# Kernel tuning notes

Measured on AMD Instinct MI355X. Metric: run time of the kernel, lower is better.

## Reference

```python
import jax, jax.numpy as jnp
import numpy as np

T, B, N = 512, 256, 128


def setup_inputs() -> dict:
    key = jax.random.key(0)
    k1, k2, k3, k4, k5, k6 = jax.random.split(key, 6)
    emit = jax.random.normal(k1, (T, B, N), dtype=jnp.float32)
    target = jax.random.randint(k2, (T, B), 0, N)
    # prefix-true mask from random lengths in [1, T]
    lengths = jax.random.randint(k3, (B,), 1, T + 1)
    mask = jnp.arange(T)[:, None] < lengths[None, :]
    std = (1.0 / N) ** 0.5
    trans = jax.random.normal(k4, (N, N), dtype=jnp.float32) * std
    strans = jax.random.normal(k5, (N,), dtype=jnp.float32) * std
    etrans = jax.random.normal(k6, (N,), dtype=jnp.float32) * std
    return {"emit": emit, "target": target, "mask": mask,
            "trans": trans, "strans": strans, "etrans": etrans}


def _logZ(emit, mask, trans, strans, etrans):
    alpha0 = strans + emit[0]  # (B, N)

    def step(alpha, xs):
        e_t, m_t = xs  # (B, N), (B,)
        # scores[b, j] = logsumexp_i(alpha[b, i] + trans[i, j] + e_t[b, j])
        scores = jax.scipy.special.logsumexp(
            alpha[:, :, None] + trans[None, :, :] + e_t[:, None, :], axis=1)
        alpha = jnp.where(m_t[:, None], scores, alpha)
        return alpha, None

    alpha, _ = jax.lax.scan(step, alpha0, (emit[1:], mask[1:]))
    return jax.scipy.special.logsumexp(alpha + etrans, axis=1).sum()


def _score(emit, target, mask, trans, strans, etrans):
    Tn, Bn, _ = emit.shape
    # emission scores of gold tags: (T, B)
    sc = jnp.take_along_axis(emit, target[:, :, None], axis=2)[..., 0]
    # transition scores between consecutive gold tags
    sc = sc.at[1:].add(trans[target[:-1], target[1:]])
    score = jnp.sum(jnp.where(mask, sc, jnp.float32(0.0)))
    ends = mask.astype(jnp.int32).sum(axis=0) - 1  # (B,)
    score = score + strans[target[0]].sum()
    score = score + etrans[target[ends, jnp.arange(Bn)]].sum()
    return score


def reference(emit, target, mask, trans, strans, etrans):
    Bn = emit.shape[1]
    logZ = _logZ(emit, mask, trans, strans, etrans)
    score = _score(emit, target, mask, trans, strans, etrans)
    return (logZ - score) / Bn
```

## Files before the change

kernel.cpp:

```cpp
#include <hip/hip_runtime.h>

#define TT 512
#define BB 256
#define NN 128
#define MW 16
#define NWG (BB / MW)
#define STH 144
#define GRID (32 + TT)

#define LENS_OFF 256
#define AF_OFF 2048
#define CF_OFF (AF_OFF + BB * NN * 4)
#define BU_OFF (CF_OFF + 1024)
#define CB_OFF (BU_OFF + BB * NN * 4)
#define WS_NEED ((size_t)CB_OFF + 1024)

typedef __attribute__((ext_vector_type(8))) short short8_t;
typedef __attribute__((ext_vector_type(4))) float f32x4;

__device__ __forceinline__ unsigned short f2bf(float f) {
  unsigned u = __float_as_uint(f);
  return (unsigned short)((u + 0x7FFF + ((u >> 16) & 1)) >> 16);
}
__device__ __forceinline__ float bf2f(unsigned short h) {
  return __uint_as_float(((unsigned)h) << 16);
}
__device__ __forceinline__ int orig_j(int p) {
  return 32 * (p >> 5) + 16 * (p & 1) + ((p >> 1) & 15);
}
__device__ __forceinline__ unsigned pk_bf16(float a, float b) {
  unsigned r;
  asm("v_cvt_pk_bf16_f32 %0, %1, %2" : "=v"(r) : "v"(a), "v"(b));
  return r;
}

#define BARRIER_LGKM() \
  asm volatile("s_waitcnt lgkmcnt(0)\n\ts_barrier" ::: "memory")

template <bool FWD>
__device__ __forceinline__ void step_one(
    int T_, bool NORM, const float* __restrict__ emit,
    unsigned short (&sVg)[2][MW * STH], int (&nrmg)[2][MW], int& nb,
    int (&cloc)[4], const int (&lm1)[4], const int (&off8)[8],
    float (&RL)[8], const float (&RO)[8], const float (&XU)[8],
    float (&XF)[8], const short8_t (&eB)[4][2], float eet0, float eet1,
    int w, int c, int qd, bool nwriter) {
  const int POUT = T_ & 1, PIN = POUT ^ 1;
  {
    int tl = FWD ? (T_ + 2 < TT ? T_ + 2 : TT - 1) : (T_ - 2 > 0 ? T_ - 2 : 0);
    const size_t gb = (size_t)tl * (BB * NN);
#pragma unroll
    for (int i = 0; i < 8; ++i) RL[i] = emit[gb + off8[i]];
  }
  const short8_t A0 = *(const short8_t*)&sVg[PIN][c * STH + 0 + qd * 8];
  const short8_t A1 = *(const short8_t*)&sVg[PIN][c * STH + 32 + qd * 8];
  const short8_t A2 = *(const short8_t*)&sVg[PIN][c * STH + 64 + qd * 8];
  const short8_t A3 = *(const short8_t*)&sVg[PIN][c * STH + 96 + qd * 8];
  f32x4 p0 = {0.f, 0.f, 0.f, 0.f}, q0 = {0.f, 0.f, 0.f, 0.f};
  f32x4 p1 = {0.f, 0.f, 0.f, 0.f}, q1 = {0.f, 0.f, 0.f, 0.f};
  p0 = __builtin_amdgcn_mfma_f32_16x16x32_bf16(A0, eB[0][0], p0, 0, 0, 0);
  p1 = __builtin_amdgcn_mfma_f32_16x16x32_bf16(A0, eB[0][1], p1, 0, 0, 0);
  q0 = __builtin_amdgcn_mfma_f32_16x16x32_bf16(A2, eB[2][0], q0, 0, 0, 0);
  q1 = __builtin_amdgcn_mfma_f32_16x16x32_bf16(A2, eB[2][1], q1, 0, 0, 0);
  p0 = __builtin_amdgcn_mfma_f32_16x16x32_bf16(A1, eB[1][0], p0, 0, 0, 0);
  p1 = __builtin_amdgcn_mfma_f32_16x16x32_bf16(A1, eB[1][1], p1, 0, 0, 0);
  q0 = __builtin_amdgcn_mfma_f32_16x16x32_bf16(A3, eB[3][0], q0, 0, 0, 0);
  q1 = __builtin_amdgcn_mfma_f32_16x16x32_bf16(A3, eB[3][1], q1, 0, 0, 0);
#pragma unroll
  for (int i = 0; i < 8; ++i) XF[i] = __expf(RO[i]);
  const f32x4 ac0 = p0 + q0;
  const f32x4 ac1 = p1 + q1;

  if (NORM) {
    const int4 nr = *(const int4*)&nrmg[nb][4 * qd];
    const int nA[4] = {nr.x, nr.y, nr.z, nr.w};
    int nnw[4];
#pragma unroll
    for (int r_ = 0; r_ < 4; ++r_) {
      float v0, v1;
      if (FWD) {
        v0 = ldexpf(ac0[r_] * XU[2 * r_], -nA[r_]);
        v1 = ldexpf(ac1[r_] * XU[2 * r_ + 1], -nA[r_]);
        if (T_ <= lm1[r_]) {
          *(unsigned*)&sVg[POUT][(4 * qd + r_) * STH + 32 * w + 2 * c] =
              pk_bf16(v0, v1);
          cloc[r_] += nA[r_];
        }
      } else {
        const bool isact = (T_ == lm1[r_]);
        v0 = isact ? XU[2 * r_] * eet0 : ldexpf(ac0[r_] * XU[2 * r_], -nA[r_]);
        v1 = isact ? XU[2 * r_ + 1] * eet1
                   : ldexpf(ac1[r_] * XU[2 * r_ + 1], -nA[r_]);
        if (T_ <= lm1[r_]) {
          *(unsigned*)&sVg[POUT][(4 * qd + r_) * STH + 32 * w + 2 * c] =
              pk_bf16(v0, v1);
          cloc[r_] = isact ? 0 : cloc[r_] + nA[r_];
        }
      }
      nnw[r_] = ((int)((__float_as_uint(v0) >> 23) & 0xFF)) - 120;
    }
    if (nwriter)
      *(int4*)&nrmg[nb ^ 1][4 * qd] = make_int4(nnw[0], nnw[1], nnw[2], nnw[3]);
    nb ^= 1;
  } else {
#pragma unroll
    for (int r_ = 0; r_ < 4; ++r_) {
      float v0, v1;
      if (FWD) {
        v0 = ac0[r_] * XU[2 * r_];
        v1 = ac1[r_] * XU[2 * r_ + 1];
        if (T_ <= lm1[r_]) {
          *(unsigned*)&sVg[POUT][(4 * qd + r_) * STH + 32 * w + 2 * c] =
              pk_bf16(v0, v1);
        }
      } else {
        const bool isact = (T_ == lm1[r_]);
        v0 = isact ? XU[2 * r_] * eet0 : ac0[r_] * XU[2 * r_];
        v1 = isact ? XU[2 * r_ + 1] * eet1 : ac1[r_] * XU[2 * r_ + 1];
        if (T_ <= lm1[r_]) {
          *(unsigned*)&sVg[POUT][(4 * qd + r_) * STH + 32 * w + 2 * c] =
              pk_bf16(v0, v1);
          cloc[r_] = isact ? 0 : cloc[r_];
        }
      }
    }
  }
}

__global__ __launch_bounds__(256, 1) void crf_fb8(
    const float* __restrict__ emit, const int* __restrict__ target,
    const void* __restrict__ maskp, const float* __restrict__ trans,
    const float* __restrict__ strans, const float* __restrict__ etrans,
    float* __restrict__ ws, int* __restrict__ lens, float* __restrict__ AF,
    int* __restrict__ CF, float* __restrict__ BU, int* __restrict__ CB) {
  __shared__ __align__(16) unsigned short sV[2][MW * STH];
  __shared__ __align__(16) int nrm[2][MW];
  __shared__ __align__(16) int sC[MW];
  __shared__ int slen[MW];
  __shared__ int smax_s;
  __shared__ float rf[4];

  const int bid = blockIdx.x;
  const int tid = threadIdx.x;
  const unsigned char* mk8 = (const unsigned char*)maskp;
  const int* mk32 = (const int*)maskp;
  const bool is_u8 = (mk8[1] != 0);

  if (bid >= 32) {
    const int b = tid;
    const int t = bid - 32;
    int m = is_u8 ? (mk8[t * BB + b] != 0) : (mk32[t * BB + b] != 0);
    float v = 0.f;
    if (m) {
      int tg = target[t * BB + b];
      v = emit[((size_t)t * BB + b) * NN + tg];
      v += (t > 0) ? trans[target[(t - 1) * BB + b] * NN + tg] : strans[tg];
      int mn = (t + 1 < TT) ? (is_u8 ? (mk8[(t + 1) * BB + b] != 0)
                                     : (mk32[(t + 1) * BB + b] != 0))
                            : 0;
      if (!mn) {
        v += etrans[tg];
        lens[b] = t + 1;
      }
    }
#pragma unroll
    for (int off = 32; off; off >>= 1) v += __shfl_down(v, off, 64);
    if ((b & 63) == 0) rf[b >> 6] = v;
    __syncthreads();
    if (b == 0) atomicAdd(&ws[1], rf[0] + rf[1] + rf[2] + rf[3]);
    return;
  }

  const bool bwd = (bid >= NWG);
  const int g = bwd ? bid - NWG : bid;
  const int bg = g * MW;
  const int w = tid >> 6, l = tid & 63, c = l & 15, qd = l >> 4;

  if (tid == 0) smax_s = 0;
  __syncthreads();
  if (tid < MW) {
    const int b = bg + tid;
    int len = 1;
#pragma unroll
    for (int st = 256; st; st >>= 1) {
      int t2 = len + st;
      if (t2 <= TT) {
        bool mv = is_u8 ? (mk8[(size_t)(t2 - 1) * BB + b] != 0)
                        : (mk32[(size_t)(t2 - 1) * BB + b] != 0);
        if (mv) len = t2;
      }
    }
    slen[tid] = len;
    atomicMax(&smax_s, len);
  }

  short8_t eB[4][2];
#pragma unroll
  for (int kt = 0; kt < 4; ++kt)
#pragma unroll
    for (int u = 0; u < 2; ++u)
#pragma unroll
      for (int jj = 0; jj < 8; ++jj) {
        int kp = kt * 32 + qd * 8 + jj;
        int a_ = orig_j(kp);
        int b_ = 32 * w + 16 * u + c;
        float tv = bwd ? trans[b_ * NN + a_] : trans[a_ * NN + b_];
        eB[kt][u][jj] = (short)f2bf(__expf(tv));
      }
  const float eet0 = __expf(etrans[32 * w + c]);
  const float eet1 = __expf(etrans[32 * w + 16 + c]);

  {
    const int m = tid & 15;
    const int pbase = (tid >> 4) * 8;
    if (!bwd) {
      const int b = bg + m;
#pragma unroll
      for (int pp = 0; pp < 8; ++pp) {
        int p = pbase + pp;
        int j = orig_j(p);
        float v = __expf(strans[j] + emit[(size_t)b * NN + j]);
        sV[0][m * STH + p] = f2bf(v);
        if (p == 0)
          nrm[0][m] = ((int)((__float_as_uint(v) >> 23) & 0xFF)) - 120;
      }
    } else {
#pragma unroll
      for (int pp = 0; pp < 8; ++pp) {
        int p = pbase + pp;
        sV[0][m * STH + p] = 0x3F80;
        sV[1][m * STH + p] = 0x3F80;
        if (p == 0) { nrm[0][m] = 0; nrm[1][m] = 0; }
      }
    }
  }
  __syncthreads();
  const int smax = smax_s;
  int lm1[4];
#pragma unroll
  for (int r = 0; r < 4; ++r) lm1[r] = slen[4 * qd + r] - 1;

  int cloc[4] = {0, 0, 0, 0};
  int nb = 0;
  const bool nwriter = (w == 0 && c == 0);

  int off8[8];
#pragma unroll
  for (int r = 0; r < 4; ++r)
#pragma unroll
    for (int u = 0; u < 2; ++u)
      off8[r * 2 + u] = (bg + 4 * qd + r) * NN + 32 * w + 16 * u + c;

  int NIT, T0;
  if (!bwd) {
    const int LmaxF = (smax < 258) ? smax : 258;
    NIT = LmaxF - 1;
    T0 = 1;
  } else {
    NIT = (smax >= 259) ? smax - 258 : 0;
    T0 = smax - 1;
  }

  if (NIT > 0) {
    float ra[8], rb[8], x0[8], x1[8];
    {
      const int a1 = bwd ? (T0 - 1 > 0 ? T0 - 1 : 0)
                         : (T0 + 1 < TT ? T0 + 1 : TT - 1);
#pragma unroll
      for (int i = 0; i < 8; ++i) {
        ra[i] = emit[(size_t)T0 * (BB * NN) + off8[i]];
        rb[i] = emit[(size_t)a1 * (BB * NN) + off8[i]];
      }
#pragma unroll
      for (int i = 0; i < 8; ++i) x0[i] = __expf(ra[i]);
    }
    if (!bwd) {
      for (int itb = 0; itb < NIT; itb += 4) {
#pragma unroll
        for (int k = 0; k < 4; ++k) {
          const int it = itb + k;
          if (it >= NIT) break;
          if ((k & 1) == 0)
            step_one<true>(T0 + it, k == 3, emit, sV, nrm, nb, cloc, lm1, off8,
                           ra, rb, x0, x1, eB, eet0, eet1, w, c, qd, nwriter);
          else
            step_one<true>(T0 + it, k == 3, emit, sV, nrm, nb, cloc, lm1, off8,
                           rb, ra, x1, x0, eB, eet0, eet1, w, c, qd, nwriter);
          BARRIER_LGKM();
        }
      }
    } else {
      for (int itb = 0; itb < NIT; itb += 4) {
#pragma unroll
        for (int k = 0; k < 4; ++k) {
          const int it = itb + k;
          if (it >= NIT) break;
          if ((k & 1) == 0)
            step_one<false>(T0 - it, k == 3, emit, sV, nrm, nb, cloc, lm1,
                            off8, ra, rb, x0, x1, eB, eet0, eet1, w, c, qd,
                            nwriter);
          else
            step_one<false>(T0 - it, k == 3, emit, sV, nrm, nb, cloc, lm1,
                            off8, rb, ra, x1, x0, eB, eet0, eet1, w, c, qd,
                            nwriter);
          BARRIER_LGKM();
        }
      }
    }
  }

  if (nwriter)
    *(int4*)&sC[4 * qd] = make_int4(cloc[0], cloc[1], cloc[2], cloc[3]);
  __syncthreads();
  {
    const int m = tid >> 4, i16 = tid & 15;
    if (!bwd) {
      int nf = slen[m] - 1;
      if (nf > 257) nf = 257;
      const int pf = nf & 1;
#pragma unroll
      for (int pp = 0; pp < 8; ++pp) {
        int p = i16 * 8 + pp;
        AF[(size_t)(bg + m) * NN + p] = bf2f(sV[pf][m * STH + p]);
      }
      if (i16 == 0) CF[bg + m] = sC[m];
    } else {
#pragma unroll
      for (int pp = 0; pp < 8; ++pp) {
        int p = i16 * 8 + pp;
        BU[(size_t)(bg + m) * NN + p] = bf2f(sV[0][m * STH + p]);
      }
      if (i16 == 0) CB[bg + m] = sC[m];
    }
  }
}

__global__ __launch_bounds__(256) void crf_comb(
    const float* __restrict__ trans, const float* __restrict__ etrans,
    const int* __restrict__ lens, const float* __restrict__ AF,
    const int* __restrict__ CF, const float* __restrict__ BU,
    const int* __restrict__ CB, float* __restrict__ ws,
    float* __restrict__ out) {
  __shared__ __align__(16) unsigned short sU[MW * STH];
  __shared__ float sRed[4][MW][2];
  __shared__ int slen[MW];
  const int tid = threadIdx.x;
  const int w = tid >> 6, l = tid & 63, c = l & 15, qd = l >> 4;
  const int g = blockIdx.x, bg = g * MW;

  if (tid < MW) slen[tid] = lens[bg + tid];
  {
    const int m = tid & 15, pbase = (tid >> 4) * 8;
#pragma unroll
    for (int pp = 0; pp < 8; ++pp) {
      int p = pbase + pp;
      sU[m * STH + p] = f2bf(BU[(size_t)(bg + m) * NN + p]);
    }
  }
  short8_t eB[4][2];
#pragma unroll
  for (int kt = 0; kt < 4; ++kt)
#pragma unroll
    for (int u = 0; u < 2; ++u)
#pragma unroll
      for (int jj = 0; jj < 8; ++jj) {
        int kp = kt * 32 + qd * 8 + jj;
        int a_ = orig_j(kp);
        int b_ = 32 * w + 16 * u + c;
        eB[kt][u][jj] = (short)f2bf(__expf(trans[b_ * NN + a_]));
      }
  const float eet0 = __expf(etrans[32 * w + c]);
  const float eet1 = __expf(etrans[32 * w + 16 + c]);
  __syncthreads();

  const short8_t A0 = *(const short8_t*)&sU[c * STH + 0 + qd * 8];
  const short8_t A1 = *(const short8_t*)&sU[c * STH + 32 + qd * 8];
  const short8_t A2 = *(const short8_t*)&sU[c * STH + 64 + qd * 8];
  const short8_t A3 = *(const short8_t*)&sU[c * STH + 96 + qd * 8];
  f32x4 ac0 = {0.f, 0.f, 0.f, 0.f}, ac1 = {0.f, 0.f, 0.f, 0.f};
  ac0 = __builtin_amdgcn_mfma_f32_16x16x32_bf16(A0, eB[0][0], ac0, 0, 0, 0);
  ac1 = __builtin_amdgcn_mfma_f32_16x16x32_bf16(A0, eB[0][1], ac1, 0, 0, 0);
  ac0 = __builtin_amdgcn_mfma_f32_16x16x32_bf16(A1, eB[1][0], ac0, 0, 0, 0);
  ac1 = __builtin_amdgcn_mfma_f32_16x16x32_bf16(A1, eB[1][1], ac1, 0, 0, 0);
  ac0 = __builtin_amdgcn_mfma_f32_16x16x32_bf16(A2, eB[2][0], ac0, 0, 0, 0);
  ac1 = __builtin_amdgcn_mfma_f32_16x16x32_bf16(A2, eB[2][1], ac1, 0, 0, 0);
  ac0 = __builtin_amdgcn_mfma_f32_16x16x32_bf16(A3, eB[3][0], ac0, 0, 0, 0);
  ac1 = __builtin_amdgcn_mfma_f32_16x16x32_bf16(A3, eB[3][1], ac1, 0, 0, 0);

#pragma unroll
  for (int r_ = 0; r_ < 4; ++r_) {
    float a0 = AF[(size_t)(bg + 4 * qd + r_) * NN + 32 * w + 2 * c];
    float a1 = AF[(size_t)(bg + 4 * qd + r_) * NN + 32 * w + 2 * c + 1];
    float dB = a0 * ac0[r_] + a1 * ac1[r_];
    float dA = a0 * eet0 + a1 * eet1;
#pragma unroll
    for (int mk = 1; mk < 16; mk <<= 1) {
      dB += __shfl_xor(dB, mk, 64);
      dA += __shfl_xor(dA, mk, 64);
    }
    if (c == 0) {
      sRed[w][4 * qd + r_][0] = dB;
      sRed[w][4 * qd + r_][1] = dA;
    }
  }
  __syncthreads();
  if (tid < MW) {
    float DB = sRed[0][tid][0] + sRed[1][tid][0] + sRed[2][tid][0] + sRed[3][tid][0];
    float DA = sRed[0][tid][1] + sRed[1][tid][1] + sRed[2][tid][1] + sRed[3][tid][1];
    const int len = slen[tid];
    const float LN2 = 0.6931471805599453f;
    float logZ;
    if (len >= 259)
      logZ = LN2 * (float)(CF[bg + tid] + CB[bg + tid]) + __logf(DB);
    else
      logZ = LN2 * (float)CF[bg + tid] + __logf(DA);
    atomicAdd(&ws[0], logZ);
  }
  __syncthreads();
  if (tid == 0) {
    __threadfence();
    unsigned old = atomicAdd((unsigned*)ws + 3, 1u);
    if (old == NWG - 1) {
      float zz = atomicAdd(&ws[0], 0.f);
      float ss = atomicAdd(&ws[1], 0.f);
      out[0] = (zz - ss) * (1.0f / (float)BB);
    }
  }
}

__global__ __launch_bounds__(256, 1) void crf_fused_fb(
    const float* __restrict__ emit, const int* __restrict__ target,
    const void* __restrict__ maskp, const float* __restrict__ trans,
    const float* __restrict__ strans, const float* __restrict__ etrans,
    float* __restrict__ ws, float* __restrict__ out) {
  __shared__ __align__(16) unsigned short sV[2][MW * STH];
  __shared__ __align__(16) int nrm[2][MW];
  __shared__ __align__(16) int sC[MW];
  __shared__ int slen[MW];
  __shared__ float sscore;
  __shared__ int smax;

  const int tid = threadIdx.x;
  const int w = tid >> 6;
  const int l = tid & 63;
  const int c = l & 15;
  const int qd = l >> 4;
  const int bg = blockIdx.x * MW;

  if (tid < MW) slen[tid] = 0;
  if (tid == 0) { sscore = 0.f; smax = 0; }
  __syncthreads();

  const unsigned char* mk8 = (const unsigned char*)maskp;
  const int* mk32 = (const int*)maskp;
  const bool is_u8 = (mk8[1] != 0);
  {
    const int mi = tid & 15;
    const int b = bg + mi;
    const int t0 = (tid >> 4) * 32;
    int cnt = 0;
    float sc = 0.f;
    for (int s = 0; s < 32; ++s) {
      int t = t0 + s;
      int m = is_u8 ? (mk8[t * BB + b] != 0) : (mk32[t * BB + b] != 0);
      if (m) {
        cnt++;
        int tg = target[t * BB + b];
        float v = emit[((size_t)t * BB + b) * NN + tg];
        v += (t > 0) ? trans[target[(t - 1) * BB + b] * NN + tg] : strans[tg];
        int mn = (t + 1 < TT) ? (is_u8 ? (mk8[(t + 1) * BB + b] != 0)
                                       : (mk32[(t + 1) * BB + b] != 0))
                              : 0;
        if (!mn) v += etrans[tg];
        sc += v;
      }
    }
    atomicAdd(&slen[mi], cnt);
    atomicAdd(&sscore, sc);
  }

  short8_t eB[4][2];
#pragma unroll
  for (int kt = 0; kt < 4; ++kt)
#pragma unroll
    for (int u = 0; u < 2; ++u)
#pragma unroll
      for (int jj = 0; jj < 8; ++jj) {
        int kp = kt * 32 + qd * 8 + jj;
        int i = orig_j(kp);
        int j = 32 * w + 16 * u + c;
        eB[kt][u][jj] = (short)f2bf(__expf(trans[i * NN + j]));
      }

  {
    const int m = tid & 15;
    const int b = bg + m;
    const int pbase = (tid >> 4) * 8;
#pragma unroll
    for (int pp = 0; pp < 8; ++pp) {
      int p = pbase + pp;
      int j = orig_j(p);
      float v = __expf(strans[j] + emit[(size_t)b * NN + j]);
      sV[0][m * STH + p] = f2bf(v);
      if (p == 0)
        nrm[0][m] = ((int)((__float_as_uint(v) >> 23) & 0xFF)) - 120;
    }
  }
  __syncthreads();

  if (tid < MW) atomicMax(&smax, slen[tid]);
  if (tid == 0) atomicAdd(&ws[1], sscore);
  __syncthreads();
  const int Lmax = smax;
  int lenr[4];
#pragma unroll
  for (int r = 0; r < 4; ++r) lenr[r] = slen[4 * qd + r];

  int off8[8];
#pragma unroll
  for (int r = 0; r < 4; ++r)
#pragma unroll
    for (int u = 0; u < 2; ++u)
      off8[r * 2 + u] = (bg + 4 * qd + r) * NN + 32 * w + 16 * u + c;

  float ra[8], rb[8], xv[8];
  {
#pragma unroll
    for (int i = 0; i < 8; ++i) ra[i] = emit[(size_t)1 * BB * NN + off8[i]];
#pragma unroll
    for (int i = 0; i < 8; ++i) rb[i] = emit[(size_t)2 * BB * NN + off8[i]];
#pragma unroll
    for (int i = 0; i < 8; ++i) xv[i] = __expf(ra[i]);
  }
  int cloc[4] = {0, 0, 0, 0};
  const bool nwriter = (w == 0 && c == 0);

#define CRF_STEP(T_, PIN, POUT, RL, RO)                                       \
  do {                                                                        \
    int tl = ((T_) + 2 < TT) ? (T_) + 2 : TT - 1;                             \
    const size_t gbase = (size_t)tl * (BB * NN);                              \
    _Pragma("unroll") for (int i_ = 0; i_ < 8; ++i_)                          \
        RL[i_] = emit[gbase + off8[i_]];                                      \
    const short8_t A0 = *(const short8_t*)&sV[PIN][c * STH + 0 + qd * 8];     \
    const short8_t A1 = *(const short8_t*)&sV[PIN][c * STH + 32 + qd * 8];    \
    const short8_t A2 = *(const short8_t*)&sV[PIN][c * STH + 64 + qd * 8];    \
    const short8_t A3 = *(const short8_t*)&sV[PIN][c * STH + 96 + qd * 8];    \
    const int4 nr = *(const int4*)&nrm[PIN][4 * qd];                          \
    f32x4 ac0 = {0.f, 0.f, 0.f, 0.f}, ac1 = {0.f, 0.f, 0.f, 0.f};             \
    ac0 = __builtin_amdgcn_mfma_f32_16x16x32_bf16(A0, eB[0][0], ac0, 0, 0, 0);\
    ac1 = __builtin_amdgcn_mfma_f32_16x16x32_bf16(A0, eB[0][1], ac1, 0, 0, 0);\
    ac0 = __builtin_amdgcn_mfma_f32_16x16x32_bf16(A1, eB[1][0], ac0, 0, 0, 0);\
    ac1 = __builtin_amdgcn_mfma_f32_16x16x32_bf16(A1, eB[1][1], ac1, 0, 0, 0);\
    ac0 = __builtin_amdgcn_mfma_f32_16x16x32_bf16(A2, eB[2][0], ac0, 0, 0, 0);\
    ac1 = __builtin_amdgcn_mfma_f32_16x16x32_bf16(A2, eB[2][1], ac1, 0, 0, 0);\
    ac0 = __builtin_amdgcn_mfma_f32_16x16x32_bf16(A3, eB[3][0], ac0, 0, 0, 0);\
    ac1 = __builtin_amdgcn_mfma_f32_16x16x32_bf16(A3, eB[3][1], ac1, 0, 0, 0);\
    const int nA[4] = {nr.x, nr.y, nr.z, nr.w};                               \
    int nnw[4];                                                               \
    _Pragma("unroll") for (int r_ = 0; r_ < 4; ++r_) {                        \
      float y0 = ac0[r_] * xv[2 * r_];                                        \
      float y1 = ac1[r_] * xv[2 * r_ + 1];                                    \
      float v0 = ldexpf(y0, -nA[r_]);                                         \
      float v1 = ldexpf(y1, -nA[r_]);                                         \
      if ((T_) < lenr[r_]) {                                                  \
        unsigned pk = (unsigned)f2bf(v0) | ((unsigned)f2bf(v1) << 16);        \
        *(unsigned*)&sV[POUT][(4 * qd + r_) * STH + 32 * w + 2 * c] = pk;     \
        cloc[r_] += nA[r_];                                                   \
      }                                                                       \
      nnw[r_] = ((int)((__float_as_uint(v0) >> 23) & 0xFF)) - 120;            \
    }                                                                         \
    if (nwriter)                                                              \
      *(int4*)&nrm[POUT][4 * qd] = make_int4(nnw[0], nnw[1], nnw[2], nnw[3]); \
    _Pragma("unroll") for (int i_ = 0; i_ < 8; ++i_)                          \
        xv[i_] = __expf(RO[i_]);                                              \
    __syncthreads();                                                          \
  } while (0)

  for (int t = 1; t < Lmax; t += 2) {
    CRF_STEP(t, 0, 1, ra, rb);
    if (t + 1 < Lmax) {
      CRF_STEP(t + 1, 1, 0, rb, ra);
    }
  }
#undef CRF_STEP

  if (nwriter) *(int4*)&sC[4 * qd] = make_int4(cloc[0], cloc[1], cloc[2], cloc[3]);
  __syncthreads();
  {
    const int m = tid >> 4, i16 = tid & 15;
    const int pb = (slen[m] - 1) & 1;
    float s = 0.f;
#pragma unroll
    for (int pp = 0; pp < 8; ++pp) {
      int p = i16 * 8 + pp;
      int j = orig_j(p);
      s += bf2f(sV[pb][m * STH + p]) * __expf(etrans[j]);
    }
    s += __shfl_xor(s, 1, 64);
    s += __shfl_xor(s, 2, 64);
    s += __shfl_xor(s, 4, 64);
    s += __shfl_xor(s, 8, 64);
    if (i16 == 0)
      atomicAdd(&ws[0], (float)sC[m] * 0.69314718f + __logf(s));
  }
  __syncthreads();
  if (tid == 0) {
    __threadfence();
    unsigned old = atomicAdd((unsigned*)ws + 3, 1u);
    if (old == NWG - 1) {
      float zz = atomicAdd(&ws[0], 0.f);
      float ss = atomicAdd(&ws[1], 0.f);
      out[0] = (zz - ss) * (1.0f / (float)BB);
    }
  }
}

extern "C" void kernel_launch(void* const* d_in, const int* in_sizes, int n_in,
                              void* d_out, int out_size, void* d_ws, size_t ws_size,
                              hipStream_t stream) {
  const float* emit = (const float*)d_in[0];
  const int* target = (const int*)d_in[1];
  const void* mask = (const void*)d_in[2];
  const float* trans = (const float*)d_in[3];
  const float* strans = (const float*)d_in[4];
  const float* etrans = (const float*)d_in[5];
  float* ws = (float*)d_ws;
  float* out = (float*)d_out;

  hipMemsetAsync(d_ws, 0, 16, stream);
  if (ws_size >= WS_NEED) {
    int* lens = (int*)((char*)d_ws + LENS_OFF);
    float* AF = (float*)((char*)d_ws + AF_OFF);
    int* CF = (int*)((char*)d_ws + CF_OFF);
    float* BU = (float*)((char*)d_ws + BU_OFF);
    int* CB = (int*)((char*)d_ws + CB_OFF);
    crf_fb8<<<GRID, 256, 0, stream>>>(emit, target, mask, trans, strans,
                                      etrans, ws, lens, AF, CF, BU, CB);
    crf_comb<<<NWG, 256, 0, stream>>>(trans, etrans, lens, AF, CF, BU, CB, ws,
                                      out);
  } else {
    crf_fused_fb<<<NWG, 256, 0, stream>>>(emit, target, mask, trans, strans,
                                          etrans, ws, out);
  }
}
```

Measured before the change: 231.2 us.

## Deepen emission prefetch to four steps and remove tail branches in recurrence loop

The forward/backward recurrence loop now rotates four emission register buffers, so global loads are issued four timesteps ahead instead of two. The iteration count is rounded up to a multiple of four, which removes the per-step break checks. Extra padded steps are made harmless by clamping the write predicate with lm1 and tmin. The normalization-exponent LDS read is hoisted out of the step function and done before the normalizing step. This aims to hide global-load latency on the serial critical path, at the cost of more registers and a few wasted padded steps.

```diff
diff --git a/kernel.cpp b/kernel.cpp
--- a/kernel.cpp
+++ b/kernel.cpp
@@ -41,13 +41,13 @@
 __device__ __forceinline__ void step_one(
     int T_, bool NORM, const float* __restrict__ emit,
     unsigned short (&sVg)[2][MW * STH], int (&nrmg)[2][MW], int& nb,
-    int (&cloc)[4], const int (&lm1)[4], const int (&off8)[8],
+    int (&cloc)[4], const int (&lm1)[4], int tmin, const int (&off8)[8],
     float (&RL)[8], const float (&RO)[8], const float (&XU)[8],
-    float (&XF)[8], const short8_t (&eB)[4][2], float eet0, float eet1,
-    int w, int c, int qd, bool nwriter) {
+    float (&XF)[8], const int4 nrPre, const short8_t (&eB)[4][2],
+    float eet0, float eet1, int w, int c, int qd, bool nwriter) {
   const int POUT = T_ & 1, PIN = POUT ^ 1;
   {
-    int tl = FWD ? (T_ + 2 < TT ? T_ + 2 : TT - 1) : (T_ - 2 > 0 ? T_ - 2 : 0);
+    int tl = FWD ? (T_ + 4 < TT ? T_ + 4 : TT - 1) : (T_ - 4 > 0 ? T_ - 4 : 0);
     const size_t gb = (size_t)tl * (BB * NN);
 #pragma unroll
     for (int i = 0; i < 8; ++i) RL[i] = emit[gb + off8[i]];
@@ -72,16 +72,16 @@
   const f32x4 ac1 = p1 + q1;
 
   if (NORM) {
-    const int4 nr = *(const int4*)&nrmg[nb][4 * qd];
-    const int nA[4] = {nr.x, nr.y, nr.z, nr.w};
+    const int nA[4] = {nrPre.x, nrPre.y, nrPre.z, nrPre.w};
     int nnw[4];
 #pragma unroll
     for (int r_ = 0; r_ < 4; ++r_) {
       float v0, v1;
+      const bool wr = (T_ <= lm1[r_]) && (T_ >= tmin);
       if (FWD) {
         v0 = ldexpf(ac0[r_] * XU[2 * r_], -nA[r_]);
         v1 = ldexpf(ac1[r_] * XU[2 * r_ + 1], -nA[r_]);
-        if (T_ <= lm1[r_]) {
+        if (wr) {
           *(unsigned*)&sVg[POUT][(4 * qd + r_) * STH + 32 * w + 2 * c] =
               pk_bf16(v0, v1);
           cloc[r_] += nA[r_];
@@ -91,7 +91,7 @@
         v0 = isact ? XU[2 * r_] * eet0 : ldexpf(ac0[r_] * XU[2 * r_], -nA[r_]);
         v1 = isact ? XU[2 * r_ + 1] * eet1
                    : ldexpf(ac1[r_] * XU[2 * r_ + 1], -nA[r_]);
-        if (T_ <= lm1[r_]) {
+        if (wr) {
           *(unsigned*)&sVg[POUT][(4 * qd + r_) * STH + 32 * w + 2 * c] =
               pk_bf16(v0, v1);
           cloc[r_] = isact ? 0 : cloc[r_] + nA[r_];
@@ -106,10 +106,11 @@
 #pragma unroll
     for (int r_ = 0; r_ < 4; ++r_) {
       float v0, v1;
+      const bool wr = (T_ <= lm1[r_]) && (T_ >= tmin);
       if (FWD) {
         v0 = ac0[r_] * XU[2 * r_];
         v1 = ac1[r_] * XU[2 * r_ + 1];
-        if (T_ <= lm1[r_]) {
+        if (wr) {
           *(unsigned*)&sVg[POUT][(4 * qd + r_) * STH + 32 * w + 2 * c] =
               pk_bf16(v0, v1);
         }
@@ -117,7 +118,7 @@
         const bool isact = (T_ == lm1[r_]);
         v0 = isact ? XU[2 * r_] * eet0 : ac0[r_] * XU[2 * r_];
         v1 = isact ? XU[2 * r_ + 1] * eet1 : ac1[r_] * XU[2 * r_ + 1];
-        if (T_ <= lm1[r_]) {
+        if (wr) {
           *(unsigned*)&sVg[POUT][(4 * qd + r_) * STH + 32 * w + 2 * c] =
               pk_bf16(v0, v1);
           cloc[r_] = isact ? 0 : cloc[r_];
@@ -127,7 +128,7 @@
   }
 }
 
-__global__ __launch_bounds__(256, 1) void crf_fb8(
+__global__ __launch_bounds__(256, 1) void crf_fb9(
     const float* __restrict__ emit, const int* __restrict__ target,
     const void* __restrict__ maskp, const float* __restrict__ trans,
     const float* __restrict__ strans, const float* __restrict__ etrans,
@@ -236,9 +237,6 @@
   }
   __syncthreads();
   const int smax = smax_s;
-  int lm1[4];
-#pragma unroll
-  for (int r = 0; r < 4; ++r) lm1[r] = slen[4 * qd + r] - 1;
 
   int cloc[4] = {0, 0, 0, 0};
   int nb = 0;
@@ -251,60 +249,85 @@
     for (int u = 0; u < 2; ++u)
       off8[r * 2 + u] = (bg + 4 * qd + r) * NN + 32 * w + 16 * u + c;
 
-  int NIT, T0;
+  int NIT, T0, tmin;
+  int lm1[4];
   if (!bwd) {
     const int LmaxF = (smax < 258) ? smax : 258;
     NIT = LmaxF - 1;
     T0 = 1;
+    tmin = 0;
+#pragma unroll
+    for (int r = 0; r < 4; ++r) {
+      int v = slen[4 * qd + r] - 1;
+      lm1[r] = v < (LmaxF - 1) ? v : (LmaxF - 1);
+    }
   } else {
     NIT = (smax >= 259) ? smax - 258 : 0;
     T0 = smax - 1;
+    tmin = 258;
+#pragma unroll
+    for (int r = 0; r < 4; ++r) lm1[r] = slen[4 * qd + r] - 1;
   }
 
   if (NIT > 0) {
-    float ra[8], rb[8], x0[8], x1[8];
+    const int NITR = (NIT + 3) & ~3;
+    float ra[8], rb[8], rc[8], rd[8], x0[8], x1[8];
     {
-      const int a1 = bwd ? (T0 - 1 > 0 ? T0 - 1 : 0)
-                         : (T0 + 1 < TT ? T0 + 1 : TT - 1);
+      const int d = bwd ? -1 : 1;
+      int t1 = T0 + d, t2 = T0 + 2 * d, t3 = T0 + 3 * d;
+      t1 = t1 < 0 ? 0 : (t1 > TT - 1 ? TT - 1 : t1);
+      t2 = t2 < 0 ? 0 : (t2 > TT - 1 ? TT - 1 : t2);
+      t3 = t3 < 0 ? 0 : (t3 > TT - 1 ? TT - 1 : t3);
 #pragma unroll
       for (int i = 0; i < 8; ++i) {
         ra[i] = emit[(size_t)T0 * (BB * NN) + off8[i]];
-        rb[i] = emit[(size_t)a1 * (BB * NN) + off8[i]];
+        rb[i] = emit[(size_t)t1 * (BB * NN) + off8[i]];
+        rc[i] = emit[(size_t)t2 * (BB * NN) + off8[i]];
+        rd[i] = emit[(size_t)t3 * (BB * NN) + off8[i]];
       }
 #pragma unroll
       for (int i = 0; i < 8; ++i) x0[i] = __expf(ra[i]);
     }
+    const int4 nrDum = make_int4(0, 0, 0, 0);
     if (!bwd) {
-      for (int itb = 0; itb < NIT; itb += 4) {
-#pragma unroll
-        for (int k = 0; k < 4; ++k) {
-          const int it = itb + k;
-          if (it >= NIT) break;
-          if ((k & 1) == 0)
-            step_one<true>(T0 + it, k == 3, emit, sV, nrm, nb, cloc, lm1, off8,
-                           ra, rb, x0, x1, eB, eet0, eet1, w, c, qd, nwriter);
-          else
-            step_one<true>(T0 + it, k == 3, emit, sV, nrm, nb, cloc, lm1, off8,
-                           rb, ra, x1, x0, eB, eet0, eet1, w, c, qd, nwriter);
-          BARRIER_LGKM();
-        }
+      for (int itb = 0; itb < NITR; itb += 4) {
+        step_one<true>(T0 + itb, false, emit, sV, nrm, nb, cloc, lm1, tmin,
+                       off8, ra, rb, x0, x1, nrDum, eB, eet0, eet1, w, c, qd,
+                       nwriter);
+        BARRIER_LGKM();
+        step_one<true>(T0 + itb + 1, false, emit, sV, nrm, nb, cloc, lm1, tmin,
+                       off8, rb, rc, x1, x0, nrDum, eB, eet0, eet1, w, c, qd,
+                       nwriter);
+        BARRIER_LGKM();
+        step_one<true>(T0 + itb + 2, false, emit, sV, nrm, nb, cloc, lm1, tmin,
+                       off8, rc, rd, x0, x1, nrDum, eB, eet0, eet1, w, c, qd,
+                       nwriter);
+        BARRIER_LGKM();
+        const int4 nrP = *(const int4*)&nrm[nb][4 * qd];
+        step_one<true>(T0 + itb + 3, true, emit, sV, nrm, nb, cloc, lm1, tmin,
+                       off8, rd, ra, x1, x0, nrP, eB, eet0, eet1, w, c, qd,
+                       nwriter);
+        BARRIER_LGKM();
       }
     } else {
-      for (int itb = 0; itb < NIT; itb += 4) {
-#pragma unroll
-        for (int k = 0; k < 4; ++k) {
-          const int it = itb + k;
-          if (it >= NIT) break;
-          if ((k & 1) == 0)
-            step_one<false>(T0 - it, k == 3, emit, sV, nrm, nb, cloc, lm1,
-                            off8, ra, rb, x0, x1, eB, eet0, eet1, w, c, qd,
-                            nwriter);
-          else
-            step_one<false>(T0 - it, k == 3, emit, sV, nrm, nb, cloc, lm1,
-                            off8, rb, ra, x1, x0, eB, eet0, eet1, w, c, qd,
-                            nwriter);
-          BARRIER_LGKM();
-        }
+      for (int itb = 0; itb < NITR; itb += 4) {
+        step_one<false>(T0 - itb, false, emit, sV, nrm, nb, cloc, lm1, tmin,
+                        off8, ra, rb, x0, x1, nrDum, eB, eet0, eet1, w, c, qd,
+                        nwriter);
+        BARRIER_LGKM();
+        step_one<false>(T0 - itb - 1, false, emit, sV, nrm, nb, cloc, lm1,
+                        tmin, off8, rb, rc, x1, x0, nrDum, eB, eet0, eet1, w,
+                        c, qd, nwriter);
+        BARRIER_LGKM();
+        step_one<false>(T0 - itb - 2, false, emit, sV, nrm, nb, cloc, lm1,
+                        tmin, off8, rc, rd, x0, x1, nrDum, eB, eet0, eet1, w,
+                        c, qd, nwriter);
+        BARRIER_LGKM();
+        const int4 nrP = *(const int4*)&nrm[nb][4 * qd];
+        step_one<false>(T0 - itb - 3, true, emit, sV, nrm, nb, cloc, lm1, tmin,
+                        off8, rd, ra, x1, x0, nrP, eB, eet0, eet1, w, c, qd,
+                        nwriter);
+        BARRIER_LGKM();
       }
     }
   }
@@ -634,7 +657,7 @@
     int* CF = (int*)((char*)d_ws + CF_OFF);
     float* BU = (float*)((char*)d_ws + BU_OFF);
     int* CB = (int*)((char*)d_ws + CB_OFF);
-    crf_fb8<<<GRID, 256, 0, stream>>>(emit, target, mask, trans, strans,
+    crf_fb9<<<GRID, 256, 0, stream>>>(emit, target, mask, trans, strans,
                                       etrans, ws, lens, AF, CF, BU, CB);
     crf_comb<<<NWG, 256, 0, stream>>>(trans, etrans, lens, AF, CF, BU, CB, ws,
                                       out);
```

Result: no change. 232.3 us (+0.5%).
